# Kernel tuning notes

Measured on AMD Instinct MI355X. Metric: run time of the kernel, lower is better.

The kernel has to match this reference:

```python
import jax, jax.numpy as jnp
import numpy as np

N, F = 8000, 256
NEG_SLOPE = 0.2


def setup_inputs() -> dict:
    key = jax.random.key(0)
    k1, k2, k3, k4, k5, k6, k7 = jax.random.split(key, 7)
    node_embeddings = jax.random.normal(k1, (N, F), dtype=jnp.float32)
    adj_matrix = jax.random.randint(k2, (N, N), 0, 2, dtype=jnp.int32)
    # Learned params: W (Linear F->F with bias), a (Linear 2F->1 with bias).
    # a's weight [1, 2F] is split into a_src (first F, applied to H_i) and
    # a_dst (last F, applied to H_j) -- mathematically identical to the
    # concat-then-linear formulation, without the N*N*2F intermediate.
    s = 1.0 / np.sqrt(F)
    W_w = jax.random.uniform(k3, (F, F), dtype=jnp.float32, minval=-s, maxval=s)
    W_b = jax.random.uniform(k4, (F,), dtype=jnp.float32, minval=-s, maxval=s)
    s2 = 1.0 / np.sqrt(2 * F)
    a_src = jax.random.uniform(k5, (F,), dtype=jnp.float32, minval=-s2, maxval=s2)
    a_dst = jax.random.uniform(k6, (F,), dtype=jnp.float32, minval=-s2, maxval=s2)
    a_b = jax.random.uniform(k7, (), dtype=jnp.float32, minval=-s2, maxval=s2)
    return {
        "node_embeddings": node_embeddings,
        "adj_matrix": adj_matrix,
        "W_w": W_w,
        "W_b": W_b,
        "a_src": a_src,
        "a_dst": a_dst,
        "a_b": a_b,
    }


def reference(node_embeddings, adj_matrix, W_w, W_b, a_src, a_dst, a_b):
    # H = W(x)
    H = node_embeddings @ W_w.T + W_b                      # [N, F]
    # e_ij = a([H_i ; H_j]) = H_i . a_src + H_j . a_dst + b
    e = (H @ a_src)[:, None] + (H @ a_dst)[None, :] + a_b  # [N, N]
    # mask BEFORE leakyrelu (as in the original), then leakyrelu, then softmax
    e = jnp.where(adj_matrix == 0, -jnp.inf, e)
    e = jnp.where(e >= 0, e, NEG_SLOPE * e)                # leakyrelu(-inf) = -inf
    attn = jax.nn.softmax(e, axis=1)                       # [N, N]
    return attn @ H                                        # [N, F]
```

## Files before the change

### kernel.cpp

```cpp
#include <hip/hip_runtime.h>

#define NN 8000
#define FD 256
#define NEG_SLOPE 0.2f
#define BM 64
#define KT 32
#define JS 4
#define CHUNK 2016

typedef __bf16 bf16;
typedef __bf16 bf16x8 __attribute__((ext_vector_type(8)));
typedef __bf16 bf16x4 __attribute__((ext_vector_type(4)));
typedef float f32x4 __attribute__((ext_vector_type(4)));

__global__ __launch_bounds__(256) void k_linear(const float* __restrict__ X,
                                                const float* __restrict__ W,
                                                const float* __restrict__ b,
                                                bf16* __restrict__ Ht,
                                                float* __restrict__ out,
                                                float* __restrict__ lg) {
    __shared__ float Xs[16][260];
    const int t = threadIdx.x;
    const int i0 = blockIdx.x * 16;
    {
        const int gt = blockIdx.x * 256 + t;
        const float4 z4 = {0.f, 0.f, 0.f, 0.f};
        float4* o4 = (float4*)out;
        #pragma unroll
        for (int k = 0; k < 4; ++k) o4[gt + k * 128000] = z4;
        if (gt < NN) lg[gt] = 0.f;
    }
    #pragma unroll
    for (int r = 0; r < 16; ++r)
        Xs[r][t] = X[(size_t)(i0 + r) * FD + t];
    __syncthreads();
    const int f = t;
    float acc[16];
    const float bf_ = b[f];
    #pragma unroll
    for (int ii = 0; ii < 16; ++ii) acc[ii] = bf_;
    for (int k4 = 0; k4 < FD / 4; ++k4) {
        const float4 w4 = *(const float4*)&W[(size_t)f * FD + k4 * 4];
        #pragma unroll
        for (int ii = 0; ii < 16; ++ii) {
            const float4 x4 = *(const float4*)&Xs[ii][k4 * 4];
            acc[ii] += x4.x * w4.x + x4.y * w4.y + x4.z * w4.z + x4.w * w4.w;
        }
    }
    bf16x8 v0, v1;
    #pragma unroll
    for (int ii = 0; ii < 8; ++ii) { v0[ii] = (bf16)acc[ii]; v1[ii] = (bf16)acc[ii + 8]; }
    *(bf16x8*)&Ht[(size_t)f * NN + i0]     = v0;
    *(bf16x8*)&Ht[(size_t)f * NN + i0 + 8] = v1;
}

__global__ __launch_bounds__(256) void k_attn_vec(const bf16* __restrict__ Ht,
                                                  const float* __restrict__ a_src,
                                                  const float* __restrict__ a_dst,
                                                  const float* __restrict__ a_b,
                                                  float* __restrict__ hs,
                                                  float* __restrict__ hd) {
    __shared__ float psh[4][64], pdh[4][64];
    const int t = threadIdx.x;
    const int li = t & 63;
    const int q = t >> 6;
    const int i = blockIdx.x * 64 + li;
    float ps = 0.f, pd = 0.f;
    #pragma unroll 8
    for (int fi = 0; fi < 64; ++fi) {
        const int f = q * 64 + fi;
        const float h = (float)Ht[(size_t)f * NN + i];
        ps += h * a_src[f];
        pd += h * a_dst[f];
    }
    psh[q][li] = ps; pdh[q][li] = pd;
    __syncthreads();
    if (q == 0) {
        ps = psh[0][li] + psh[1][li] + psh[2][li] + psh[3][li];
        pd = pdh[0][li] + pdh[1][li] + pdh[2][li] + pdh[3][li];
        hs[i] = ps + a_b[0];
        hd[i] = pd;
    }
}

__global__ __launch_bounds__(512, 4) void k_gat(const bf16* __restrict__ Ht,
                                                const int* __restrict__ adj,
                                                const float* __restrict__ hs,
                                                const float* __restrict__ hd,
                                                float* __restrict__ out,
                                                float* __restrict__ lg) {
    __shared__ __attribute__((aligned(16))) bf16 Bt[2][FD * KT];
    __shared__ __attribute__((aligned(16))) bf16 Wt[2][BM * KT];

    const int t  = threadIdx.x;
    const int l  = t & 63;
    const int wv = t >> 6;
    const int ib = blockIdx.x >> 2;
    const int jb = blockIdx.x & 3;
    const int i0 = ib * BM;
    const int jq0 = jb * CHUNK;
    const int NS = (jb < 3) ? 63 : 61;

    const int r  = t >> 3;
    const int jm = (t & 7) << 2;
    const float hsv = hs[i0 + r];
    const int* adjp  = adj + (size_t)(i0 + r) * NN + jq0 + jm;
    const float* hdp = hd + jq0 + jm;
    const int woff = r * 64 + (((jm >> 3) ^ ((r >> 2) & 3)) << 4) + (((jm >> 2) & 1) << 3);

    const int al = l & 15, asl = l >> 4;
    const int eff = (asl ^ ((al >> 2) & 3)) << 4;

    auto stage = [&](int s_, int bufi) {
        #pragma unroll
        for (int q = 0; q < 2; ++q) {
            const int idx = q * 512 + t;
            const int col = idx >> 2;
            const int kk = (idx & 3) ^ ((col >> 2) & 3);
            const bf16* src = Ht + (size_t)col * NN + jq0 + s_ * KT + kk * 8;
            bf16* dst = &Bt[bufi][(q * 512 + wv * 64) * 8];
            __builtin_amdgcn_global_load_lds(
                (const __attribute__((address_space(1))) void*)src,
                (__attribute__((address_space(3))) void*)dst, 16, 0, 0);
        }
    };

    int4   adjc = *(const int4*)adjp;
    float4 hdc  = *(const float4*)hdp;
    stage(0, 0);

    f32x4 acc[4][2];
    #pragma unroll
    for (int sr = 0; sr < 4; ++sr) {
        acc[sr][0] = (f32x4){0.f, 0.f, 0.f, 0.f};
        acc[sr][1] = (f32x4){0.f, 0.f, 0.f, 0.f};
    }
    float lsum = 0.f;

    #pragma unroll 1
    for (int s = 0; s < NS; ++s) {
        const int cur = s & 1;
        int4 adjn; float4 hdn;
        if (s + 1 < NS) {
            adjn = *(const int4*)(adjp + (size_t)(s + 1) * KT);
            hdn  = *(const float4*)(hdp + (size_t)(s + 1) * KT);
            stage(s + 1, cur ^ 1);
        }

        {
            float e, w0, w1, w2, w3;
            e = hsv + hdc.x; e = e >= 0.f ? e : NEG_SLOPE * e; w0 = adjc.x ? __expf(e) : 0.f;
            e = hsv + hdc.y; e = e >= 0.f ? e : NEG_SLOPE * e; w1 = adjc.y ? __expf(e) : 0.f;
            e = hsv + hdc.z; e = e >= 0.f ? e : NEG_SLOPE * e; w2 = adjc.z ? __expf(e) : 0.f;
            e = hsv + hdc.w; e = e >= 0.f ? e : NEG_SLOPE * e; w3 = adjc.w ? __expf(e) : 0.f;
            lsum += (w0 + w1) + (w2 + w3);
            bf16x4 wp; wp[0] = (bf16)w0; wp[1] = (bf16)w1; wp[2] = (bf16)w2; wp[3] = (bf16)w3;
            *(bf16x4*)((char*)&Wt[cur][0] + woff) = wp;
        }

        if (s + 1 < NS) asm volatile("s_waitcnt vmcnt(4)" ::: "memory");
        else            asm volatile("s_waitcnt vmcnt(0)" ::: "memory");
        asm volatile("s_waitcnt lgkmcnt(0)" ::: "memory");
        __builtin_amdgcn_s_barrier();

        {
            const char* wb = (const char*)&Wt[cur][0];
            const char* bb = (const char*)&Bt[cur][0];
            bf16x8 a[4], b[2];
            #pragma unroll
            for (int sr = 0; sr < 4; ++sr)
                a[sr] = *(const bf16x8*)(wb + (sr * 16 + al) * 64 + eff);
            #pragma unroll
            for (int cf = 0; cf < 2; ++cf)
                b[cf] = *(const bf16x8*)(bb + (wv * 32 + cf * 16 + al) * 64 + eff);
            #pragma unroll
            for (int sr = 0; sr < 4; ++sr) {
                acc[sr][0] = __builtin_amdgcn_mfma_f32_16x16x32_bf16(a[sr], b[0], acc[sr][0], 0, 0, 0);
                acc[sr][1] = __builtin_amdgcn_mfma_f32_16x16x32_bf16(a[sr], b[1], acc[sr][1], 0, 0, 0);
            }
        }
        asm volatile("s_waitcnt lgkmcnt(0)" ::: "memory");
        __builtin_amdgcn_s_barrier();

        adjc = adjn; hdc = hdn;
    }

    lsum += __shfl_xor(lsum, 1);
    lsum += __shfl_xor(lsum, 2);
    lsum += __shfl_xor(lsum, 4);
    if ((t & 7) == 0) atomicAdd(&lg[i0 + r], lsum);

    #pragma unroll
    for (int sr = 0; sr < 4; ++sr) {
        #pragma unroll
        for (int cf = 0; cf < 2; ++cf) {
            #pragma unroll
            for (int g = 0; g < 4; ++g) {
                atomicAdd(&out[(size_t)(i0 + sr * 16 + asl * 4 + g) * FD + wv * 32 + cf * 16 + al],
                          acc[sr][cf][g]);
            }
        }
    }
}

__global__ __launch_bounds__(256) void k_norm(float* __restrict__ out,
                                              const float* __restrict__ lg) {
    const int i = blockIdx.x;
    const float rinv = 1.0f / lg[i];
    out[(size_t)i * FD + threadIdx.x] *= rinv;
}

extern "C" void kernel_launch(void* const* d_in, const int* in_sizes, int n_in,
                              void* d_out, int out_size, void* d_ws, size_t ws_size,
                              hipStream_t stream) {
    const float* X     = (const float*)d_in[0];
    const int*   adj   = (const int*)d_in[1];
    const float* Ww    = (const float*)d_in[2];
    const float* Wb    = (const float*)d_in[3];
    const float* a_src = (const float*)d_in[4];
    const float* a_dst = (const float*)d_in[5];
    const float* a_b   = (const float*)d_in[6];
    float* out = (float*)d_out;

    bf16*  Ht = (bf16*)d_ws;
    float* hs = (float*)((char*)d_ws + (size_t)FD * NN * sizeof(bf16));
    float* hd = hs + NN;
    float* lg = hd + NN;

    k_linear<<<NN / 16, 256, 0, stream>>>(X, Ww, Wb, Ht, out, lg);
    k_attn_vec<<<NN / 64, 256, 0, stream>>>(Ht, a_src, a_dst, a_b, hs, hd);
    k_gat<<<(NN / BM) * JS, 512, 0, stream>>>(Ht, adj, hs, hd, out, lg);
    k_norm<<<NN, 256, 0, stream>>>(out, lg);
}
```

Baseline: 150.9 us.

## Restructure GAT kernel to compute transposed output with weights in registers

The attention-aggregation kernel is reorganized so each wave generates its attention weights directly in registers as the MFMA B operand, which removes the shared-memory weight tile and one barrier per step. Ht tiles are staged into LDS at a doubled K depth of 64 with an XOR swizzle, and each wave accumulates all 256 feature columns for 16 rows. The result is written transposed into a workspace buffer via atomics, and the normalization kernel now also transposes back through shared memory. The aim is fewer barriers and LDS traffic per MFMA, at the cost of more accumulator registers (16 f32x4), lower thread count per block, and an extra transpose pass.

```diff
diff --git a/kernel.cpp b/kernel.cpp
--- a/kernel.cpp
+++ b/kernel.cpp
@@ -3,21 +3,19 @@
 #define NN 8000
 #define FD 256
 #define NEG_SLOPE 0.2f
-#define BM 64
-#define KT 32
+#define BI 64
+#define KT 64
 #define JS 4
-#define CHUNK 2016
 
 typedef __bf16 bf16;
 typedef __bf16 bf16x8 __attribute__((ext_vector_type(8)));
-typedef __bf16 bf16x4 __attribute__((ext_vector_type(4)));
 typedef float f32x4 __attribute__((ext_vector_type(4)));
 
 __global__ __launch_bounds__(256) void k_linear(const float* __restrict__ X,
                                                 const float* __restrict__ W,
                                                 const float* __restrict__ b,
                                                 bf16* __restrict__ Ht,
-                                                float* __restrict__ out,
+                                                float* __restrict__ outT,
                                                 float* __restrict__ lg) {
     __shared__ float Xs[16][260];
     const int t = threadIdx.x;
@@ -25,7 +23,7 @@
     {
         const int gt = blockIdx.x * 256 + t;
         const float4 z4 = {0.f, 0.f, 0.f, 0.f};
-        float4* o4 = (float4*)out;
+        float4* o4 = (float4*)outT;
         #pragma unroll
         for (int k = 0; k < 4; ++k) o4[gt + k * 128000] = z4;
         if (gt < NN) lg[gt] = 0.f;
@@ -83,131 +81,143 @@
     }
 }
 
-__global__ __launch_bounds__(512, 4) void k_gat(const bf16* __restrict__ Ht,
+__device__ __forceinline__ bf16x8 wgen(int4 alo, int4 ahi, float4 hlo, float4 hhi,
+                                       float hsv, float& ls) {
+    float w[8]; float e;
+    e = hsv + hlo.x; e = e >= 0.f ? e : NEG_SLOPE * e; w[0] = alo.x ? __expf(e) : 0.f;
+    e = hsv + hlo.y; e = e >= 0.f ? e : NEG_SLOPE * e; w[1] = alo.y ? __expf(e) : 0.f;
+    e = hsv + hlo.z; e = e >= 0.f ? e : NEG_SLOPE * e; w[2] = alo.z ? __expf(e) : 0.f;
+    e = hsv + hlo.w; e = e >= 0.f ? e : NEG_SLOPE * e; w[3] = alo.w ? __expf(e) : 0.f;
+    e = hsv + hhi.x; e = e >= 0.f ? e : NEG_SLOPE * e; w[4] = ahi.x ? __expf(e) : 0.f;
+    e = hsv + hhi.y; e = e >= 0.f ? e : NEG_SLOPE * e; w[5] = ahi.y ? __expf(e) : 0.f;
+    e = hsv + hhi.z; e = e >= 0.f ? e : NEG_SLOPE * e; w[6] = ahi.z ? __expf(e) : 0.f;
+    e = hsv + hhi.w; e = e >= 0.f ? e : NEG_SLOPE * e; w[7] = ahi.w ? __expf(e) : 0.f;
+    ls += ((w[0] + w[1]) + (w[2] + w[3])) + ((w[4] + w[5]) + (w[6] + w[7]));
+    bf16x8 r;
+    #pragma unroll
+    for (int i = 0; i < 8; ++i) r[i] = (bf16)w[i];
+    return r;
+}
+
+__global__ __launch_bounds__(256, 2) void k_gat(const bf16* __restrict__ Ht,
                                                 const int* __restrict__ adj,
                                                 const float* __restrict__ hs,
                                                 const float* __restrict__ hd,
-                                                float* __restrict__ out,
+                                                float* __restrict__ outT,
                                                 float* __restrict__ lg) {
-    __shared__ __attribute__((aligned(16))) bf16 Bt[2][FD * KT];
-    __shared__ __attribute__((aligned(16))) bf16 Wt[2][BM * KT];
+    __shared__ __attribute__((aligned(16))) bf16 As[2][FD * KT];
 
     const int t  = threadIdx.x;
     const int l  = t & 63;
     const int wv = t >> 6;
     const int ib = blockIdx.x >> 2;
     const int jb = blockIdx.x & 3;
-    const int i0 = ib * BM;
-    const int jq0 = jb * CHUNK;
-    const int NS = (jb < 3) ? 63 : 61;
-
-    const int r  = t >> 3;
-    const int jm = (t & 7) << 2;
-    const float hsv = hs[i0 + r];
-    const int* adjp  = adj + (size_t)(i0 + r) * NN + jq0 + jm;
-    const float* hdp = hd + jq0 + jm;
-    const int woff = r * 64 + (((jm >> 3) ^ ((r >> 2) & 3)) << 4) + (((jm >> 2) & 1) << 3);
+    const int i0 = ib * BI;
+    const int jq0 = jb * 2048;
+    const int NS = (jb < 3) ? 32 : 29;
 
     const int al = l & 15, asl = l >> 4;
-    const int eff = (asl ^ ((al >> 2) & 3)) << 4;
+    const int i = i0 + wv * 16 + al;
+    const float hsv = hs[i];
+    const int*   adjp = adj + (size_t)i * NN + jq0 + asl * 8;
+    const float* hdp  = hd + jq0 + asl * 8;
 
     auto stage = [&](int s_, int bufi) {
         #pragma unroll
-        for (int q = 0; q < 2; ++q) {
-            const int idx = q * 512 + t;
-            const int col = idx >> 2;
-            const int kk = (idx & 3) ^ ((col >> 2) & 3);
-            const bf16* src = Ht + (size_t)col * NN + jq0 + s_ * KT + kk * 8;
-            bf16* dst = &Bt[bufi][(q * 512 + wv * 64) * 8];
+        for (int q = 0; q < 8; ++q) {
+            const int idx = q * 256 + t;
+            const int row = idx >> 3;
+            const int sslot = (idx & 7) ^ (row & 7);
+            const bf16* src = Ht + (size_t)row * NN + jq0 + s_ * KT + sslot * 8;
+            bf16* dst = &As[bufi][idx * 8];
             __builtin_amdgcn_global_load_lds(
                 (const __attribute__((address_space(1))) void*)src,
                 (__attribute__((address_space(3))) void*)dst, 16, 0, 0);
         }
     };
 
-    int4   adjc = *(const int4*)adjp;
-    float4 hdc  = *(const float4*)hdp;
     stage(0, 0);
-
-    f32x4 acc[4][2];
-    #pragma unroll
-    for (int sr = 0; sr < 4; ++sr) {
-        acc[sr][0] = (f32x4){0.f, 0.f, 0.f, 0.f};
-        acc[sr][1] = (f32x4){0.f, 0.f, 0.f, 0.f};
-    }
+    int4 aj0 = *(const int4*)adjp,        aj1 = *(const int4*)(adjp + 4);
+    int4 aj2 = *(const int4*)(adjp + 32), aj3 = *(const int4*)(adjp + 36);
+    float4 hc0 = *(const float4*)hdp,        hc1 = *(const float4*)(hdp + 4);
+    float4 hc2 = *(const float4*)(hdp + 32), hc3 = *(const float4*)(hdp + 36);
+
+    f32x4 acc[16];
+    #pragma unroll
+    for (int ff = 0; ff < 16; ++ff) acc[ff] = (f32x4){0.f, 0.f, 0.f, 0.f};
     float lsum = 0.f;
 
     #pragma unroll 1
     for (int s = 0; s < NS; ++s) {
         const int cur = s & 1;
-        int4 adjn; float4 hdn;
+        int4 na0, na1, na2, na3; float4 nh0, nh1, nh2, nh3;
         if (s + 1 < NS) {
-            adjn = *(const int4*)(adjp + (size_t)(s + 1) * KT);
-            hdn  = *(const float4*)(hdp + (size_t)(s + 1) * KT);
             stage(s + 1, cur ^ 1);
-        }
+            const int o = (s + 1) * KT;
+            na0 = *(const int4*)(adjp + o);      na1 = *(const int4*)(adjp + o + 4);
+            na2 = *(const int4*)(adjp + o + 32); na3 = *(const int4*)(adjp + o + 36);
+            nh0 = *(const float4*)(hdp + o);      nh1 = *(const float4*)(hdp + o + 4);
+            nh2 = *(const float4*)(hdp + o + 32); nh3 = *(const float4*)(hdp + o + 36);
+        }
+
+        const bf16x8 b0 = wgen(aj0, aj1, hc0, hc1, hsv, lsum);
+        const bf16x8 b1 = wgen(aj2, aj3, hc2, hc3, hsv, lsum);
+
+        if (s + 1 < NS) asm volatile("s_waitcnt vmcnt(16)" ::: "memory");
+        else            asm volatile("s_waitcnt vmcnt(0)" ::: "memory");
+        __builtin_amdgcn_s_barrier();
 
         {
-            float e, w0, w1, w2, w3;
-            e = hsv + hdc.x; e = e >= 0.f ? e : NEG_SLOPE * e; w0 = adjc.x ? __expf(e) : 0.f;
-            e = hsv + hdc.y; e = e >= 0.f ? e : NEG_SLOPE * e; w1 = adjc.y ? __expf(e) : 0.f;
-            e = hsv + hdc.z; e = e >= 0.f ? e : NEG_SLOPE * e; w2 = adjc.z ? __expf(e) : 0.f;
-            e = hsv + hdc.w; e = e >= 0.f ? e : NEG_SLOPE * e; w3 = adjc.w ? __expf(e) : 0.f;
-            lsum += (w0 + w1) + (w2 + w3);
-            bf16x4 wp; wp[0] = (bf16)w0; wp[1] = (bf16)w1; wp[2] = (bf16)w2; wp[3] = (bf16)w3;
-            *(bf16x4*)((char*)&Wt[cur][0] + woff) = wp;
-        }
-
-        if (s + 1 < NS) asm volatile("s_waitcnt vmcnt(4)" ::: "memory");
-        else            asm volatile("s_waitcnt vmcnt(0)" ::: "memory");
+            const char* Ab = (const char*)&As[cur][0];
+            #pragma unroll
+            for (int ff = 0; ff < 16; ++ff) {
+                const int rb = (ff * 16 + al) * 128;
+                const bf16x8 a0 = *(const bf16x8*)(Ab + rb + ((asl ^ (al & 7)) << 4));
+                const bf16x8 a1 = *(const bf16x8*)(Ab + rb + (((4 + asl) ^ (al & 7)) << 4));
+                acc[ff] = __builtin_amdgcn_mfma_f32_16x16x32_bf16(a0, b0, acc[ff], 0, 0, 0);
+                acc[ff] = __builtin_amdgcn_mfma_f32_16x16x32_bf16(a1, b1, acc[ff], 0, 0, 0);
+            }
+        }
         asm volatile("s_waitcnt lgkmcnt(0)" ::: "memory");
         __builtin_amdgcn_s_barrier();
 
-        {
-            const char* wb = (const char*)&Wt[cur][0];
-            const char* bb = (const char*)&Bt[cur][0];
-            bf16x8 a[4], b[2];
-            #pragma unroll
-            for (int sr = 0; sr < 4; ++sr)
-                a[sr] = *(const bf16x8*)(wb + (sr * 16 + al) * 64 + eff);
-            #pragma unroll
-            for (int cf = 0; cf < 2; ++cf)
-                b[cf] = *(const bf16x8*)(bb + (wv * 32 + cf * 16 + al) * 64 + eff);
-            #pragma unroll
-            for (int sr = 0; sr < 4; ++sr) {
-                acc[sr][0] = __builtin_amdgcn_mfma_f32_16x16x32_bf16(a[sr], b[0], acc[sr][0], 0, 0, 0);
-                acc[sr][1] = __builtin_amdgcn_mfma_f32_16x16x32_bf16(a[sr], b[1], acc[sr][1], 0, 0, 0);
-            }
-        }
-        asm volatile("s_waitcnt lgkmcnt(0)" ::: "memory");
-        __builtin_amdgcn_s_barrier();
-
-        adjc = adjn; hdc = hdn;
-    }
-
-    lsum += __shfl_xor(lsum, 1);
-    lsum += __shfl_xor(lsum, 2);
-    lsum += __shfl_xor(lsum, 4);
-    if ((t & 7) == 0) atomicAdd(&lg[i0 + r], lsum);
-
-    #pragma unroll
-    for (int sr = 0; sr < 4; ++sr) {
-        #pragma unroll
-        for (int cf = 0; cf < 2; ++cf) {
-            #pragma unroll
-            for (int g = 0; g < 4; ++g) {
-                atomicAdd(&out[(size_t)(i0 + sr * 16 + asl * 4 + g) * FD + wv * 32 + cf * 16 + al],
-                          acc[sr][cf][g]);
-            }
-        }
-    }
-}
-
-__global__ __launch_bounds__(256) void k_norm(float* __restrict__ out,
-                                              const float* __restrict__ lg) {
-    const int i = blockIdx.x;
-    const float rinv = 1.0f / lg[i];
-    out[(size_t)i * FD + threadIdx.x] *= rinv;
+        aj0 = na0; aj1 = na1; aj2 = na2; aj3 = na3;
+        hc0 = nh0; hc1 = nh1; hc2 = nh2; hc3 = nh3;
+    }
+
+    lsum += __shfl_xor(lsum, 16);
+    lsum += __shfl_xor(lsum, 32);
+    if (asl == 0) atomicAdd(&lg[i], lsum);
+
+    #pragma unroll
+    for (int ff = 0; ff < 16; ++ff) {
+        #pragma unroll
+        for (int g = 0; g < 4; ++g) {
+            atomicAdd(&outT[(size_t)(ff * 16 + asl * 4 + g) * NN + i], acc[ff][g]);
+        }
+    }
+}
+
+__global__ __launch_bounds__(256) void k_norm(const float* __restrict__ outT,
+                                              const float* __restrict__ lg,
+                                              float* __restrict__ out) {
+    __shared__ float Ts[64][65];
+    const int t = threadIdx.x;
+    const int tx = t & 63, ty = t >> 6;
+    const int ib = blockIdx.x >> 2, fb = blockIdx.x & 3;
+    const int i0 = ib * 64, f0 = fb * 64;
+    #pragma unroll
+    for (int r = 0; r < 16; ++r) {
+        const int f = ty * 16 + r;
+        Ts[f][tx] = outT[(size_t)(f0 + f) * NN + i0 + tx];
+    }
+    __syncthreads();
+    #pragma unroll
+    for (int r = 0; r < 16; ++r) {
+        const int irow = ty * 16 + r;
+        const float rinv = 1.0f / lg[i0 + irow];
+        out[(size_t)(i0 + irow) * FD + f0 + tx] = Ts[tx][irow] * rinv;
+    }
 }
 
 extern "C" void kernel_launch(void* const* d_in, const int* in_sizes, int n_in,
@@ -222,13 +232,14 @@
     const float* a_b   = (const float*)d_in[6];
     float* out = (float*)d_out;
 
-    bf16*  Ht = (bf16*)d_ws;
-    float* hs = (float*)((char*)d_ws + (size_t)FD * NN * sizeof(bf16));
-    float* hd = hs + NN;
-    float* lg = hd + NN;
-
-    k_linear<<<NN / 16, 256, 0, stream>>>(X, Ww, Wb, Ht, out, lg);
+    bf16*  Ht   = (bf16*)d_ws;
+    float* hs   = (float*)((char*)d_ws + (size_t)FD * NN * sizeof(bf16));
+    float* hd   = hs + NN;
+    float* lg   = hd + NN;
+    float* outT = lg + NN;
+
+    k_linear<<<NN / 16, 256, 0, stream>>>(X, Ww, Wb, Ht, outT, lg);
     k_attn_vec<<<NN / 64, 256, 0, stream>>>(Ht, a_src, a_dst, a_b, hs, hd);
-    k_gat<<<(NN / BM) * JS, 512, 0, stream>>>(Ht, adj, hs, hd, out, lg);
-    k_norm<<<NN, 256, 0, stream>>>(out, lg);
-}
+    k_gat<<<(NN / BI) * JS, 256, 0, stream>>>(Ht, adj, hs, hd, outT, lg);
+    k_norm<<<(NN / 64) * (FD / 64), 256, 0, stream>>>(outT, lg, out);
+}
```

After: 155.2 us. +2.8%, slower.

## Split fused attention-weight generation and PV matmul into separate kernels

Applied to the files above, without the earlier changes.

Splits the fused GAT kernel in two. A streaming kernel computes masked exp weights into a bf16 N×NNP matrix and accumulates row sums, and a separate MFMA GEMM multiplies that matrix by H. H is padded to a stride of 8064 columns with zeroed tail, and the GEMM reads H fragments directly from global memory while staging the weight tile in LDS. This aims to decouple the adjacency/exp stream from the matmul pipeline. In exchange it adds a roughly 129 MB bf16 intermediate that is written and then read back.

```diff
diff --git a/kernel.cpp b/kernel.cpp
--- a/kernel.cpp
+++ b/kernel.cpp
@@ -1,16 +1,12 @@
 #include <hip/hip_runtime.h>
 
 #define NN 8000
+#define NNP 8064
 #define FD 256
 #define NEG_SLOPE 0.2f
-#define BM 64
-#define KT 32
-#define JS 4
-#define CHUNK 2016
 
 typedef __bf16 bf16;
 typedef __bf16 bf16x8 __attribute__((ext_vector_type(8)));
-typedef __bf16 bf16x4 __attribute__((ext_vector_type(4)));
 typedef float f32x4 __attribute__((ext_vector_type(4)));
 
 __global__ __launch_bounds__(256) void k_linear(const float* __restrict__ X,
@@ -29,6 +25,10 @@
         #pragma unroll
         for (int k = 0; k < 4; ++k) o4[gt + k * 128000] = z4;
         if (gt < NN) lg[gt] = 0.f;
+        if (gt < FD * 8) {
+            const int f = gt >> 3, p = gt & 7;
+            *(int4*)&Ht[(size_t)f * NNP + NN + p * 8] = (int4){0, 0, 0, 0};
+        }
     }
     #pragma unroll
     for (int r = 0; r < 16; ++r)
@@ -50,8 +50,8 @@
     bf16x8 v0, v1;
     #pragma unroll
     for (int ii = 0; ii < 8; ++ii) { v0[ii] = (bf16)acc[ii]; v1[ii] = (bf16)acc[ii + 8]; }
-    *(bf16x8*)&Ht[(size_t)f * NN + i0]     = v0;
-    *(bf16x8*)&Ht[(size_t)f * NN + i0 + 8] = v1;
+    *(bf16x8*)&Ht[(size_t)f * NNP + i0]     = v0;
+    *(bf16x8*)&Ht[(size_t)f * NNP + i0 + 8] = v1;
 }
 
 __global__ __launch_bounds__(256) void k_attn_vec(const bf16* __restrict__ Ht,
@@ -69,7 +69,7 @@
     #pragma unroll 8
     for (int fi = 0; fi < 64; ++fi) {
         const int f = q * 64 + fi;
-        const float h = (float)Ht[(size_t)f * NN + i];
+        const float h = (float)Ht[(size_t)f * NNP + i];
         ps += h * a_src[f];
         pd += h * a_dst[f];
     }
@@ -83,121 +83,145 @@
     }
 }
 
-__global__ __launch_bounds__(512, 4) void k_gat(const bf16* __restrict__ Ht,
-                                                const int* __restrict__ adj,
-                                                const float* __restrict__ hs,
-                                                const float* __restrict__ hd,
-                                                float* __restrict__ out,
-                                                float* __restrict__ lg) {
-    __shared__ __attribute__((aligned(16))) bf16 Bt[2][FD * KT];
-    __shared__ __attribute__((aligned(16))) bf16 Wt[2][BM * KT];
+__device__ __forceinline__ bf16x8 wgen8(int4 alo, int4 ahi, float4 hlo, float4 hhi,
+                                        float hsv, float& ls) {
+    float w[8]; float e;
+    e = hsv + hlo.x; e = fmaxf(e, NEG_SLOPE * e); w[0] = alo.x ? __expf(e) : 0.f;
+    e = hsv + hlo.y; e = fmaxf(e, NEG_SLOPE * e); w[1] = alo.y ? __expf(e) : 0.f;
+    e = hsv + hlo.z; e = fmaxf(e, NEG_SLOPE * e); w[2] = alo.z ? __expf(e) : 0.f;
+    e = hsv + hlo.w; e = fmaxf(e, NEG_SLOPE * e); w[3] = alo.w ? __expf(e) : 0.f;
+    e = hsv + hhi.x; e = fmaxf(e, NEG_SLOPE * e); w[4] = ahi.x ? __expf(e) : 0.f;
+    e = hsv + hhi.y; e = fmaxf(e, NEG_SLOPE * e); w[5] = ahi.y ? __expf(e) : 0.f;
+    e = hsv + hhi.z; e = fmaxf(e, NEG_SLOPE * e); w[6] = ahi.z ? __expf(e) : 0.f;
+    e = hsv + hhi.w; e = fmaxf(e, NEG_SLOPE * e); w[7] = ahi.w ? __expf(e) : 0.f;
+    ls += ((w[0] + w[1]) + (w[2] + w[3])) + ((w[4] + w[5]) + (w[6] + w[7]));
+    bf16x8 r;
+    #pragma unroll
+    for (int i = 0; i < 8; ++i) r[i] = (bf16)w[i];
+    return r;
+}
+
+__global__ __launch_bounds__(256) void k_wgen(const int* __restrict__ adj,
+                                              const float* __restrict__ hs,
+                                              const float* __restrict__ hd,
+                                              bf16* __restrict__ Wm,
+                                              float* __restrict__ lg) {
+    const int t = threadIdx.x;
+    const int l = t & 63;
+    const int wid = blockIdx.x * 4 + (t >> 6);
+    const int nw = gridDim.x * 4;
+    const int r = l >> 3, sl = l & 7;
+    const int NT = 1000 * 126;
+    for (int tau = wid; tau < NT; tau += nw) {
+        const int ig = tau / 126;
+        const int jt = tau - ig * 126;
+        const int i = ig * 8 + r;
+        const int j0 = jt * 64 + sl * 8;
+        bf16* wp = Wm + (size_t)i * NNP + j0;
+        if (jt == 125) {
+            *(int4*)wp = (int4){0, 0, 0, 0};
+            continue;
+        }
+        const int4 a0 = *(const int4*)(adj + (size_t)i * NN + j0);
+        const int4 a1 = *(const int4*)(adj + (size_t)i * NN + j0 + 4);
+        const float4 h0 = *(const float4*)(hd + j0);
+        const float4 h1 = *(const float4*)(hd + j0 + 4);
+        const float hsv = hs[i];
+        float ls = 0.f;
+        const bf16x8 w8 = wgen8(a0, a1, h0, h1, hsv, ls);
+        *(bf16x8*)wp = w8;
+        ls += __shfl_xor(ls, 1);
+        ls += __shfl_xor(ls, 2);
+        ls += __shfl_xor(ls, 4);
+        if (sl == 0) atomicAdd(&lg[i], ls);
+    }
+}
+
+__global__ __launch_bounds__(256, 4) void k_pv(const bf16* __restrict__ Wm,
+                                               const bf16* __restrict__ Ht,
+                                               float* __restrict__ out) {
+    __shared__ __attribute__((aligned(16))) bf16 As[2][64 * 64];
 
     const int t  = threadIdx.x;
     const int l  = t & 63;
-    const int wv = t >> 6;
-    const int ib = blockIdx.x >> 2;
-    const int jb = blockIdx.x & 3;
-    const int i0 = ib * BM;
-    const int jq0 = jb * CHUNK;
-    const int NS = (jb < 3) ? 63 : 61;
-
-    const int r  = t >> 3;
-    const int jm = (t & 7) << 2;
-    const float hsv = hs[i0 + r];
-    const int* adjp  = adj + (size_t)(i0 + r) * NN + jq0 + jm;
-    const float* hdp = hd + jq0 + jm;
-    const int woff = r * 64 + (((jm >> 3) ^ ((r >> 2) & 3)) << 4) + (((jm >> 2) & 1) << 3);
+    const int fq = t >> 6;
+    const int ib = blockIdx.x % 125;
+    const int jb = blockIdx.x / 125;
+    const int i0 = ib * 64;
+    const int jq0 = jb * 1024;
+    const int NS = (jb < 7) ? 16 : 14;
 
     const int al = l & 15, asl = l >> 4;
-    const int eff = (asl ^ ((al >> 2) & 3)) << 4;
+    const int swz = al & 7;
 
     auto stage = [&](int s_, int bufi) {
         #pragma unroll
         for (int q = 0; q < 2; ++q) {
-            const int idx = q * 512 + t;
-            const int col = idx >> 2;
-            const int kk = (idx & 3) ^ ((col >> 2) & 3);
-            const bf16* src = Ht + (size_t)col * NN + jq0 + s_ * KT + kk * 8;
-            bf16* dst = &Bt[bufi][(q * 512 + wv * 64) * 8];
+            const int idx = q * 256 + t;
+            const int row = idx >> 3;
+            const int slot = idx & 7;
+            const bf16* src = Wm + (size_t)(i0 + row) * NNP + jq0 + s_ * 64
+                              + ((slot ^ (row & 7)) * 8);
+            bf16* dst = &As[bufi][idx * 8];
             __builtin_amdgcn_global_load_lds(
                 (const __attribute__((address_space(1))) void*)src,
                 (__attribute__((address_space(3))) void*)dst, 16, 0, 0);
         }
     };
 
-    int4   adjc = *(const int4*)adjp;
-    float4 hdc  = *(const float4*)hdp;
     stage(0, 0);
 
-    f32x4 acc[4][2];
-    #pragma unroll
-    for (int sr = 0; sr < 4; ++sr) {
-        acc[sr][0] = (f32x4){0.f, 0.f, 0.f, 0.f};
-        acc[sr][1] = (f32x4){0.f, 0.f, 0.f, 0.f};
-    }
-    float lsum = 0.f;
+    const bf16* htb = Ht + (size_t)(fq * 64 + al) * NNP + jq0 + asl * 8;
+
+    f32x4 acc[4][4];
+    #pragma unroll
+    for (int rf = 0; rf < 4; ++rf)
+        #pragma unroll
+        for (int cf = 0; cf < 4; ++cf) acc[rf][cf] = (f32x4){0.f, 0.f, 0.f, 0.f};
 
     #pragma unroll 1
     for (int s = 0; s < NS; ++s) {
         const int cur = s & 1;
-        int4 adjn; float4 hdn;
-        if (s + 1 < NS) {
-            adjn = *(const int4*)(adjp + (size_t)(s + 1) * KT);
-            hdn  = *(const float4*)(hdp + (size_t)(s + 1) * KT);
-            stage(s + 1, cur ^ 1);
-        }
-
-        {
-            float e, w0, w1, w2, w3;
-            e = hsv + hdc.x; e = e >= 0.f ? e : NEG_SLOPE * e; w0 = adjc.x ? __expf(e) : 0.f;
-            e = hsv + hdc.y; e = e >= 0.f ? e : NEG_SLOPE * e; w1 = adjc.y ? __expf(e) : 0.f;
-            e = hsv + hdc.z; e = e >= 0.f ? e : NEG_SLOPE * e; w2 = adjc.z ? __expf(e) : 0.f;
-            e = hsv + hdc.w; e = e >= 0.f ? e : NEG_SLOPE * e; w3 = adjc.w ? __expf(e) : 0.f;
-            lsum += (w0 + w1) + (w2 + w3);
-            bf16x4 wp; wp[0] = (bf16)w0; wp[1] = (bf16)w1; wp[2] = (bf16)w2; wp[3] = (bf16)w3;
-            *(bf16x4*)((char*)&Wt[cur][0] + woff) = wp;
-        }
-
-        if (s + 1 < NS) asm volatile("s_waitcnt vmcnt(4)" ::: "memory");
+
+        bf16x8 bfr[2][4];
+        #pragma unroll
+        for (int kk = 0; kk < 2; ++kk)
+            #pragma unroll
+            for (int cf = 0; cf < 4; ++cf)
+                bfr[kk][cf] = *(const bf16x8*)(htb + (size_t)cf * 16 * NNP + s * 64 + kk * 32);
+        __builtin_amdgcn_sched_barrier(0);
+        if (s + 1 < NS) stage(s + 1, cur ^ 1);
+
+        if (s + 1 < NS) asm volatile("s_waitcnt vmcnt(10)" ::: "memory");
         else            asm volatile("s_waitcnt vmcnt(0)" ::: "memory");
+        __builtin_amdgcn_s_barrier();
+
+        const char* Ab = (const char*)&As[cur][0];
+        #pragma unroll
+        for (int kk = 0; kk < 2; ++kk) {
+            #pragma unroll
+            for (int rf = 0; rf < 4; ++rf) {
+                const int row = rf * 16 + al;
+                const bf16x8 a = *(const bf16x8*)(Ab + row * 128 +
+                                                  (((kk * 4 + asl) ^ swz) << 4));
+                acc[rf][0] = __builtin_amdgcn_mfma_f32_16x16x32_bf16(a, bfr[kk][0], acc[rf][0], 0, 0, 0);
+                acc[rf][1] = __builtin_amdgcn_mfma_f32_16x16x32_bf16(a, bfr[kk][1], acc[rf][1], 0, 0, 0);
+                acc[rf][2] = __builtin_amdgcn_mfma_f32_16x16x32_bf16(a, bfr[kk][2], acc[rf][2], 0, 0, 0);
+                acc[rf][3] = __builtin_amdgcn_mfma_f32_16x16x32_bf16(a, bfr[kk][3], acc[rf][3], 0, 0, 0);
+            }
+        }
         asm volatile("s_waitcnt lgkmcnt(0)" ::: "memory");
         __builtin_amdgcn_s_barrier();
-
-        {
-            const char* wb = (const char*)&Wt[cur][0];
-            const char* bb = (const char*)&Bt[cur][0];
-            bf16x8 a[4], b[2];
-            #pragma unroll
-            for (int sr = 0; sr < 4; ++sr)
-                a[sr] = *(const bf16x8*)(wb + (sr * 16 + al) * 64 + eff);
-            #pragma unroll
-            for (int cf = 0; cf < 2; ++cf)
-                b[cf] = *(const bf16x8*)(bb + (wv * 32 + cf * 16 + al) * 64 + eff);
-            #pragma unroll
-            for (int sr = 0; sr < 4; ++sr) {
-                acc[sr][0] = __builtin_amdgcn_mfma_f32_16x16x32_bf16(a[sr], b[0], acc[sr][0], 0, 0, 0);
-                acc[sr][1] = __builtin_amdgcn_mfma_f32_16x16x32_bf16(a[sr], b[1], acc[sr][1], 0, 0, 0);
-            }
-        }
-        asm volatile("s_waitcnt lgkmcnt(0)" ::: "memory");
-        __builtin_amdgcn_s_barrier();
-
-        adjc = adjn; hdc = hdn;
-    }
-
-    lsum += __shfl_xor(lsum, 1);
-    lsum += __shfl_xor(lsum, 2);
-    lsum += __shfl_xor(lsum, 4);
-    if ((t & 7) == 0) atomicAdd(&lg[i0 + r], lsum);
-
-    #pragma unroll
-    for (int sr = 0; sr < 4; ++sr) {
-        #pragma unroll
-        for (int cf = 0; cf < 2; ++cf) {
+    }
+
+    #pragma unroll
+    for (int rf = 0; rf < 4; ++rf) {
+        #pragma unroll
+        for (int cf = 0; cf < 4; ++cf) {
             #pragma unroll
             for (int g = 0; g < 4; ++g) {
-                atomicAdd(&out[(size_t)(i0 + sr * 16 + asl * 4 + g) * FD + wv * 32 + cf * 16 + al],
-                          acc[sr][cf][g]);
+                atomicAdd(&out[(size_t)(i0 + rf * 16 + asl * 4 + g) * FD
+                               + fq * 64 + cf * 16 + al], acc[rf][cf][g]);
             }
         }
     }
@@ -223,12 +247,14 @@
     float* out = (float*)d_out;
 
     bf16*  Ht = (bf16*)d_ws;
-    float* hs = (float*)((char*)d_ws + (size_t)FD * NN * sizeof(bf16));
+    float* hs = (float*)((char*)d_ws + (size_t)FD * NNP * sizeof(bf16));
     float* hd = hs + NN;
     float* lg = hd + NN;
+    bf16*  Wm = (bf16*)(lg + NN);
 
     k_linear<<<NN / 16, 256, 0, stream>>>(X, Ww, Wb, Ht, out, lg);
     k_attn_vec<<<NN / 64, 256, 0, stream>>>(Ht, a_src, a_dst, a_b, hs, hd);
-    k_gat<<<(NN / BM) * JS, 512, 0, stream>>>(Ht, adj, hs, hd, out, lg);
+    k_wgen<<<2048, 256, 0, stream>>>(adj, hs, hd, Wm, lg);
+    k_pv<<<125 * 8, 256, 0, stream>>>(Wm, Ht, out);
     k_norm<<<NN, 256, 0, stream>>>(out, lg);
 }
```

After: 233.9 us. +55.0%, slower.

## Pack adjacency into bitmask and widen GAT K-tile to 64

Applied to the files above, without the earlier changes.

Adds a pre-pass kernel that packs the int32 adjacency matrix into 64-bit ballot bitmasks, so the main attention kernel reads one bit per edge instead of four bytes. The GAT kernel's K tile grows from 32 to 64 with a new XOR-swizzled LDS layout, a single weight buffer, and a 2x4 MFMA tiling per wave. The main loop is no longer software-pipelined for the mask and hd loads. The full 256MB adjacency is still read once in the pack kernel, so the gain relies on that pass running at streaming bandwidth and the GAT loop becoming cheaper.

```diff
diff --git a/kernel.cpp b/kernel.cpp
--- a/kernel.cpp
+++ b/kernel.cpp
@@ -4,14 +4,35 @@
 #define FD 256
 #define NEG_SLOPE 0.2f
 #define BM 64
-#define KT 32
-#define JS 4
-#define CHUNK 2016
+#define KT 64
+#define BSTRIDE 128
 
 typedef __bf16 bf16;
 typedef __bf16 bf16x8 __attribute__((ext_vector_type(8)));
-typedef __bf16 bf16x4 __attribute__((ext_vector_type(4)));
 typedef float f32x4 __attribute__((ext_vector_type(4)));
+typedef unsigned long long u64;
+
+__global__ __launch_bounds__(256) void k_pack(const int* __restrict__ adj,
+                                              u64* __restrict__ bits) {
+    const int l = threadIdx.x & 63;
+    const int i = blockIdx.x * 4 + (threadIdx.x >> 6);
+    const int* ap = adj + (size_t)i * NN + l;
+    u64* bp = bits + (size_t)i * BSTRIDE;
+    #pragma unroll 1
+    for (int k8 = 0; k8 < 16; ++k8) {
+        u64 myw = 0;
+        #pragma unroll
+        for (int sub = 0; sub < 8; ++sub) {
+            const int w = k8 * 8 + sub;
+            if (w < 125) {
+                const int a = ap[(size_t)w * 64];
+                const u64 m = __ballot(a != 0);
+                if (l == sub) myw = m;
+            }
+        }
+        if (l < 8 && (k8 * 8 + l) < 125) bp[k8 * 8 + l] = myw;
+    }
+}
 
 __global__ __launch_bounds__(256) void k_linear(const float* __restrict__ X,
                                                 const float* __restrict__ W,
@@ -84,13 +105,13 @@
 }
 
 __global__ __launch_bounds__(512, 4) void k_gat(const bf16* __restrict__ Ht,
-                                                const int* __restrict__ adj,
+                                                const u64* __restrict__ bits,
                                                 const float* __restrict__ hs,
                                                 const float* __restrict__ hd,
                                                 float* __restrict__ out,
                                                 float* __restrict__ lg) {
     __shared__ __attribute__((aligned(16))) bf16 Bt[2][FD * KT];
-    __shared__ __attribute__((aligned(16))) bf16 Wt[2][BM * KT];
+    __shared__ __attribute__((aligned(16))) bf16 Wt[BM * KT];
 
     const int t  = threadIdx.x;
     const int l  = t & 63;
@@ -98,64 +119,70 @@
     const int ib = blockIdx.x >> 2;
     const int jb = blockIdx.x & 3;
     const int i0 = ib * BM;
-    const int jq0 = jb * CHUNK;
-    const int NS = (jb < 3) ? 63 : 61;
+    const int jq0 = jb * 2048;
+    const int NS = (jb < 3) ? 32 : 29;
 
     const int r  = t >> 3;
-    const int jm = (t & 7) << 2;
+    const int b8 = t & 7;
+    const int jm = b8 * 8;
     const float hsv = hs[i0 + r];
-    const int* adjp  = adj + (size_t)(i0 + r) * NN + jq0 + jm;
+    const u64* brow = bits + (size_t)(i0 + r) * BSTRIDE + (jq0 >> 6);
     const float* hdp = hd + jq0 + jm;
-    const int woff = r * 64 + (((jm >> 3) ^ ((r >> 2) & 3)) << 4) + (((jm >> 2) & 1) << 3);
-
+    const int woff = r * KT + ((b8 ^ (r & 7)) << 3);
+
+    const int rh = wv >> 2, cg = wv & 3;
     const int al = l & 15, asl = l >> 4;
-    const int eff = (asl ^ ((al >> 2) & 3)) << 4;
 
     auto stage = [&](int s_, int bufi) {
         #pragma unroll
-        for (int q = 0; q < 2; ++q) {
+        for (int q = 0; q < 4; ++q) {
             const int idx = q * 512 + t;
-            const int col = idx >> 2;
-            const int kk = (idx & 3) ^ ((col >> 2) & 3);
-            const bf16* src = Ht + (size_t)col * NN + jq0 + s_ * KT + kk * 8;
-            bf16* dst = &Bt[bufi][(q * 512 + wv * 64) * 8];
+            const int col = idx >> 3;
+            const int slot = idx & 7;
+            const bf16* src = Ht + (size_t)col * NN + jq0 + s_ * KT
+                              + ((slot ^ (col & 7)) * 8);
+            bf16* dst = &Bt[bufi][idx * 8];
             __builtin_amdgcn_global_load_lds(
                 (const __attribute__((address_space(1))) void*)src,
                 (__attribute__((address_space(3))) void*)dst, 16, 0, 0);
         }
     };
 
-    int4   adjc = *(const int4*)adjp;
-    float4 hdc  = *(const float4*)hdp;
     stage(0, 0);
 
-    f32x4 acc[4][2];
-    #pragma unroll
-    for (int sr = 0; sr < 4; ++sr) {
-        acc[sr][0] = (f32x4){0.f, 0.f, 0.f, 0.f};
-        acc[sr][1] = (f32x4){0.f, 0.f, 0.f, 0.f};
-    }
+    f32x4 acc[2][4];
+    #pragma unroll
+    for (int rb = 0; rb < 2; ++rb)
+        #pragma unroll
+        for (int cf = 0; cf < 4; ++cf) acc[rb][cf] = (f32x4){0.f, 0.f, 0.f, 0.f};
     float lsum = 0.f;
 
     #pragma unroll 1
     for (int s = 0; s < NS; ++s) {
         const int cur = s & 1;
-        int4 adjn; float4 hdn;
-        if (s + 1 < NS) {
-            adjn = *(const int4*)(adjp + (size_t)(s + 1) * KT);
-            hdn  = *(const float4*)(hdp + (size_t)(s + 1) * KT);
-            stage(s + 1, cur ^ 1);
-        }
+
+        const u64 word = brow[s];
+        const float4 h0 = *(const float4*)(hdp + s * 64);
+        const float4 h1 = *(const float4*)(hdp + s * 64 + 4);
+        __builtin_amdgcn_sched_barrier(0);
+        if (s + 1 < NS) stage(s + 1, cur ^ 1);
 
         {
-            float e, w0, w1, w2, w3;
-            e = hsv + hdc.x; e = e >= 0.f ? e : NEG_SLOPE * e; w0 = adjc.x ? __expf(e) : 0.f;
-            e = hsv + hdc.y; e = e >= 0.f ? e : NEG_SLOPE * e; w1 = adjc.y ? __expf(e) : 0.f;
-            e = hsv + hdc.z; e = e >= 0.f ? e : NEG_SLOPE * e; w2 = adjc.z ? __expf(e) : 0.f;
-            e = hsv + hdc.w; e = e >= 0.f ? e : NEG_SLOPE * e; w3 = adjc.w ? __expf(e) : 0.f;
-            lsum += (w0 + w1) + (w2 + w3);
-            bf16x4 wp; wp[0] = (bf16)w0; wp[1] = (bf16)w1; wp[2] = (bf16)w2; wp[3] = (bf16)w3;
-            *(bf16x4*)((char*)&Wt[cur][0] + woff) = wp;
+            const unsigned int byte = (unsigned int)((word >> jm) & 0xffULL);
+            float w[8]; float e;
+            e = hsv + h0.x; e = fmaxf(e, NEG_SLOPE * e); w[0] = (byte & 1)   ? __expf(e) : 0.f;
+            e = hsv + h0.y; e = fmaxf(e, NEG_SLOPE * e); w[1] = (byte & 2)   ? __expf(e) : 0.f;
+            e = hsv + h0.z; e = fmaxf(e, NEG_SLOPE * e); w[2] = (byte & 4)   ? __expf(e) : 0.f;
+            e = hsv + h0.w; e = fmaxf(e, NEG_SLOPE * e); w[3] = (byte & 8)   ? __expf(e) : 0.f;
+            e = hsv + h1.x; e = fmaxf(e, NEG_SLOPE * e); w[4] = (byte & 16)  ? __expf(e) : 0.f;
+            e = hsv + h1.y; e = fmaxf(e, NEG_SLOPE * e); w[5] = (byte & 32)  ? __expf(e) : 0.f;
+            e = hsv + h1.z; e = fmaxf(e, NEG_SLOPE * e); w[6] = (byte & 64)  ? __expf(e) : 0.f;
+            e = hsv + h1.w; e = fmaxf(e, NEG_SLOPE * e); w[7] = (byte & 128) ? __expf(e) : 0.f;
+            lsum += ((w[0] + w[1]) + (w[2] + w[3])) + ((w[4] + w[5]) + (w[6] + w[7]));
+            bf16x8 w8;
+            #pragma unroll
+            for (int e2 = 0; e2 < 8; ++e2) w8[e2] = (bf16)w[e2];
+            *(bf16x8*)&Wt[woff] = w8;
         }
 
         if (s + 1 < NS) asm volatile("s_waitcnt vmcnt(4)" ::: "memory");
@@ -164,25 +191,35 @@
         __builtin_amdgcn_s_barrier();
 
         {
-            const char* wb = (const char*)&Wt[cur][0];
-            const char* bb = (const char*)&Bt[cur][0];
-            bf16x8 a[4], b[2];
-            #pragma unroll
-            for (int sr = 0; sr < 4; ++sr)
-                a[sr] = *(const bf16x8*)(wb + (sr * 16 + al) * 64 + eff);
-            #pragma unroll
-            for (int cf = 0; cf < 2; ++cf)
-                b[cf] = *(const bf16x8*)(bb + (wv * 32 + cf * 16 + al) * 64 + eff);
-            #pragma unroll
-            for (int sr = 0; sr < 4; ++sr) {
-                acc[sr][0] = __builtin_amdgcn_mfma_f32_16x16x32_bf16(a[sr], b[0], acc[sr][0], 0, 0, 0);
-                acc[sr][1] = __builtin_amdgcn_mfma_f32_16x16x32_bf16(a[sr], b[1], acc[sr][1], 0, 0, 0);
+            const char* Ab = (const char*)Wt;
+            const char* Bb = (const char*)&Bt[cur][0];
+            bf16x8 a[2][2], bb[4][2];
+            #pragma unroll
+            for (int rb = 0; rb < 2; ++rb) {
+                const int row = rh * 32 + rb * 16 + al;
+                #pragma unroll
+                for (int kh = 0; kh < 2; ++kh)
+                    a[rb][kh] = *(const bf16x8*)(Ab + row * 128 +
+                                                 (((kh * 4 + asl) ^ (row & 7)) << 4));
             }
+            #pragma unroll
+            for (int cf = 0; cf < 4; ++cf) {
+                const int col = cg * 64 + cf * 16 + al;
+                #pragma unroll
+                for (int kh = 0; kh < 2; ++kh)
+                    bb[cf][kh] = *(const bf16x8*)(Bb + col * 128 +
+                                                  (((kh * 4 + asl) ^ (col & 7)) << 4));
+            }
+            #pragma unroll
+            for (int rb = 0; rb < 2; ++rb)
+                #pragma unroll
+                for (int cf = 0; cf < 4; ++cf) {
+                    acc[rb][cf] = __builtin_amdgcn_mfma_f32_16x16x32_bf16(a[rb][0], bb[cf][0], acc[rb][cf], 0, 0, 0);
+                    acc[rb][cf] = __builtin_amdgcn_mfma_f32_16x16x32_bf16(a[rb][1], bb[cf][1], acc[rb][cf], 0, 0, 0);
+                }
         }
         asm volatile("s_waitcnt lgkmcnt(0)" ::: "memory");
         __builtin_amdgcn_s_barrier();
-
-        adjc = adjn; hdc = hdn;
     }
 
     lsum += __shfl_xor(lsum, 1);
@@ -191,16 +228,13 @@
     if ((t & 7) == 0) atomicAdd(&lg[i0 + r], lsum);
 
     #pragma unroll
-    for (int sr = 0; sr < 4; ++sr) {
-        #pragma unroll
-        for (int cf = 0; cf < 2; ++cf) {
-            #pragma unroll
-            for (int g = 0; g < 4; ++g) {
-                atomicAdd(&out[(size_t)(i0 + sr * 16 + asl * 4 + g) * FD + wv * 32 + cf * 16 + al],
-                          acc[sr][cf][g]);
-            }
-        }
-    }
+    for (int rb = 0; rb < 2; ++rb)
+        #pragma unroll
+        for (int cf = 0; cf < 4; ++cf)
+            #pragma unroll
+            for (int g = 0; g < 4; ++g)
+                atomicAdd(&out[(size_t)(i0 + rh * 32 + rb * 16 + asl * 4 + g) * FD
+                               + cg * 64 + cf * 16 + al], acc[rb][cf][g]);
 }
 
 __global__ __launch_bounds__(256) void k_norm(float* __restrict__ out,
@@ -222,13 +256,15 @@
     const float* a_b   = (const float*)d_in[6];
     float* out = (float*)d_out;
 
-    bf16*  Ht = (bf16*)d_ws;
-    float* hs = (float*)((char*)d_ws + (size_t)FD * NN * sizeof(bf16));
-    float* hd = hs + NN;
-    float* lg = hd + NN;
-
+    bf16*  Ht   = (bf16*)d_ws;
+    float* hs   = (float*)((char*)d_ws + (size_t)FD * NN * sizeof(bf16));
+    float* hd   = hs + NN;
+    float* lg   = hd + NN;
+    u64*   bits = (u64*)(lg + NN + 8);
+
+    k_pack<<<NN / 4, 256, 0, stream>>>(adj, bits);
     k_linear<<<NN / 16, 256, 0, stream>>>(X, Ww, Wb, Ht, out, lg);
     k_attn_vec<<<NN / 64, 256, 0, stream>>>(Ht, a_src, a_dst, a_b, hs, hd);
-    k_gat<<<(NN / BM) * JS, 512, 0, stream>>>(Ht, adj, hs, hd, out, lg);
+    k_gat<<<(NN / BM) * 4, 512, 0, stream>>>(Ht, bits, hs, hd, out, lg);
     k_norm<<<NN, 256, 0, stream>>>(out, lg);
 }
```

Result: slower. 159.9 us (+6.0%).
